# Performance work log

Hardware: AMD Instinct MI355X
Metric: run time of the kernel (lower is better)

The kernel has to match this reference:

```python
import jax, jax.numpy as jnp
import numpy as np

D = 1024  # encoder_output_size

def setup_inputs() -> dict:
    key = jax.random.key(0)
    ks = jax.random.split(key, 5)
    scale = 1.0 / np.sqrt(D)  # roughly matches nn.Linear init spread
    seq = jax.random.normal(ks[0], (2048, 8, D), dtype=jnp.float32)
    Kw1 = jax.random.normal(ks[1], (D, D), dtype=jnp.float32) * scale
    Kw2 = jax.random.normal(ks[2], (D, D), dtype=jnp.float32) * scale
    Qw1 = jax.random.normal(ks[3], (D, D), dtype=jnp.float32) * scale
    Qw2 = jax.random.normal(ks[4], (D, D), dtype=jnp.float32) * scale
    return {"sequence": seq, "Kw1": Kw1, "Kw2": Kw2, "Qw1": Qw1, "Qw2": Qw2}

def _mlp(x, W1, W2):
    # nn.Linear(bias=False): y = x @ W^T ; tanh after each
    return jnp.tanh(jnp.tanh(x @ W1.T) @ W2.T)

def reference(sequence, Kw1, Kw2, Qw1, Qw2):
    x = jnp.transpose(sequence, (1, 0, 2))          # [B, S, D]
    keys = _mlp(x, Kw1, Kw2)                        # [B, S, D]
    queries = _mlp(x, Qw1, Qw2)                     # [B, S, D]
    scale = 1.0 / jnp.sqrt(jnp.float32(x.shape[-1]))
    weights = jnp.einsum('bsd,btd->bst', keys, queries) * scale  # [B, S, S]
    weights = jax.nn.softmax(weights, axis=-1)
    attended = jnp.einsum('bst,btd->bsd', weights, x)            # [B, S, D]
    return jnp.transpose(attended, (1, 0, 2))       # [S, B, D]
```

## Files before the change

### kernel.cpp

```cpp
#include <hip/hip_runtime.h>
#include <hip/hip_bf16.h>

#define SEQ 2048
#define NB 8
#define DIM 1024

typedef __attribute__((ext_vector_type(4))) float f32x4;
typedef __attribute__((ext_vector_type(8))) short bf16x8;
typedef __attribute__((ext_vector_type(4))) unsigned short u16x4;

__device__ __forceinline__ unsigned short f2bf(float f) {
    __hip_bfloat16 h = __float2bfloat16(f);
    return *reinterpret_cast<unsigned short*>(&h);
}
__device__ __forceinline__ float bf2f(unsigned short u) {
    union { unsigned u; float f; } x; x.u = ((unsigned)u) << 16;
    return x.f;
}
__device__ __forceinline__ float fast_tanh(float x) {
    float e = __expf(x + x);
    float r = __builtin_amdgcn_rcpf(e + 1.0f);
    return fmaf(-2.0f, r, 1.0f);
}

__global__ __launch_bounds__(256) void convert_w4(const float* __restrict__ kw1,
                                                  const float* __restrict__ kw2,
                                                  const float* __restrict__ qw1,
                                                  const float* __restrict__ qw2,
                                                  unsigned short* __restrict__ out) {
    int sel = blockIdx.y;
    const float* src = sel == 0 ? kw1 : (sel == 1 ? qw1 : (sel == 2 ? kw2 : qw2));
    int i = blockIdx.x * 256 + threadIdx.x;
    float4 v = reinterpret_cast<const float4*>(src)[i];
    u16x4 o = { f2bf(v.x), f2bf(v.y), f2bf(v.z), f2bf(v.w) };
    reinterpret_cast<u16x4*>(out + (size_t)sel * DIM * DIM)[i] = o;
}

__global__ __launch_bounds__(256) void make_xb(const float* __restrict__ seq,
                                               unsigned short* __restrict__ xb) {
    int sb = blockIdx.x;
    int s = sb >> 3, b = sb & 7;
    const float4* src = reinterpret_cast<const float4*>(seq + (size_t)sb * DIM);
    u16x4* dst = reinterpret_cast<u16x4*>(xb + ((size_t)b * SEQ + s) * DIM);
    int t = threadIdx.x;
    float4 v = src[t];
    u16x4 o = { f2bf(v.x), f2bf(v.y), f2bf(v.z), f2bf(v.w) };
    dst[t] = o;
}

__global__ __launch_bounds__(256) void make_xbT(const float* __restrict__ seq,
                                                unsigned short* __restrict__ xbT) {
    __shared__ unsigned short tile[64][65];
    int s0 = blockIdx.x * 64, d0 = blockIdx.y * 64, b = blockIdx.z;
    int t = threadIdx.x;
    int dx = (t & 15) * 4, sy = t >> 4;
    #pragma unroll
    for (int i = 0; i < 4; ++i) {
        int s = s0 + sy + i * 16;
        float4 v = *reinterpret_cast<const float4*>(seq + ((size_t)s * NB + b) * DIM + d0 + dx);
        tile[sy + i * 16][dx + 0] = f2bf(v.x);
        tile[sy + i * 16][dx + 1] = f2bf(v.y);
        tile[sy + i * 16][dx + 2] = f2bf(v.z);
        tile[sy + i * 16][dx + 3] = f2bf(v.w);
    }
    __syncthreads();
    int sx = (t & 15) * 4, dy = t >> 4;
    #pragma unroll
    for (int i = 0; i < 4; ++i) {
        int d = d0 + dy + i * 16;
        u16x4 o = { tile[sx + 0][dy + i * 16], tile[sx + 1][dy + i * 16],
                    tile[sx + 2][dy + i * 16], tile[sx + 3][dy + i * 16] };
        *reinterpret_cast<u16x4*>(xbT + ((size_t)b * DIM + d) * SEQ + s0 + sx) = o;
    }
}

__global__ __launch_bounds__(256) void zero_rowsum(float* __restrict__ rs) {
    rs[blockIdx.x * 256 + threadIdx.x] = 0.0f;
}

__device__ __forceinline__ void gload16(const unsigned short* g, unsigned short* l) {
    __builtin_amdgcn_global_load_lds((const __attribute__((address_space(1))) void*)g,
                                     (__attribute__((address_space(3))) void*)l,
                                     16, 0, 0);
}

#define MFMA16(I0, J0)                                                                            \
    _Pragma("unroll")                                                                             \
    for (int ks = 0; ks < 2; ++ks)                                                                \
        _Pragma("unroll")                                                                         \
        for (int ii = 0; ii < 4; ++ii)                                                            \
            _Pragma("unroll")                                                                     \
            for (int jj = 0; jj < 2; ++jj)                                                        \
                acc[I0 + ii][J0 + jj] = __builtin_amdgcn_mfma_f32_16x16x32_bf16(                   \
                    a[I0 + ii][ks], b[J0 + jj][ks], acc[I0 + ii][J0 + jj], 0, 0, 0);

template<int MODE>
__global__ __launch_bounds__(512, 2) void gemm256(
    const unsigned short* __restrict__ A, size_t sA, int lda,
    const unsigned short* __restrict__ B, size_t sB, int ldb,
    void* __restrict__ Cv, size_t sC, int ldc,
    int K, float scale, float* __restrict__ rowsum)
{
    __shared__ unsigned short AsF[2 * 2 * 8192];
    __shared__ unsigned short BsF[2 * 2 * 8192];

    const int gx = gridDim.x, gy = gridDim.y;
    const int nwg = gx * gy * gridDim.z;
    const int fid = blockIdx.x + gx * (blockIdx.y + gy * blockIdx.z);
    const int cpx = nwg >> 3;
    const int sw = (fid & 7) * cpx + (fid >> 3);
    const int bx = sw % gx;
    const int rem = sw / gx;
    const int by = rem % gy;
    const int bz = rem / gy;

    const unsigned short* Ab = A + sA * bz;
    const unsigned short* Bb = B + sB * bz;
    const int m0 = by * 256;
    const int n0 = bx * 256;

    const int t_ = threadIdx.x;
    const int lane = t_ & 63;
    const int w = t_ >> 6;
    const int wm = w >> 2;
    const int wn = w & 3;

    const int l3 = lane >> 3;
    const int g7 = lane & 7;
    const size_t h128a = (size_t)128 * lda, r8a = (size_t)8 * lda;
    const size_t h128b = (size_t)128 * ldb, r8b = (size_t)8 * ldb;
    const unsigned short* gA = Ab + (size_t)(m0 + w * 16 + l3) * lda + ((g7 ^ l3) << 3);
    const unsigned short* gB = Bb + (size_t)(n0 + w * 16 + l3) * ldb + ((g7 ^ l3) << 3);

    const int fr = lane & 15;
    const int hi4 = lane >> 4;
    const int off0 = fr * 64 + (((hi4) ^ g7) << 3);
    const int off1 = fr * 64 + (((4 + hi4) ^ g7) << 3);
    const int bno = (wn & 1) * 4096;
    const int wlds = w * 1024;

    f32x4 acc[8][4] = {};
    const int NT = K >> 6;

    gload16(gA, AsF + wlds);                     gload16(gA + r8a, AsF + wlds + 512);
    gload16(gA + h128a, AsF + 8192 + wlds);      gload16(gA + h128a + r8a, AsF + 8192 + wlds + 512);
    gload16(gB, BsF + wlds);                     gload16(gB + r8b, BsF + wlds + 512);
    gload16(gB + h128b, BsF + 8192 + wlds);      gload16(gB + h128b + r8b, BsF + 8192 + wlds + 512);
    {
        const unsigned short* gb1 = gB + 64;
        gload16(gb1, BsF + 16384 + wlds);                gload16(gb1 + r8b, BsF + 16384 + wlds + 512);
        gload16(gb1 + h128b, BsF + 16384 + 8192 + wlds); gload16(gb1 + h128b + r8b, BsF + 16384 + 8192 + wlds + 512);
    }
    asm volatile("s_waitcnt vmcnt(4)" ::: "memory");
    __builtin_amdgcn_s_barrier();

    const unsigned short* gA1 = gA + 64;
    const unsigned short* gB2 = gB + 128;

    for (int u = 0; u < NT; ++u) {
        const int bu = (u & 1) * 16384;
        const int bn = 16384 - bu;
        const unsigned short* pA = AsF + bu + wm * 8192;
        const unsigned short* pB = BsF + bu + (wn >> 1) * 8192 + bno;
        const bool pfA = (u + 1 < NT);
        const bool pfB = (u + 2 < NT);
        bf16x8 a[8][2], b[4][2];

        #pragma unroll
        for (int i = 0; i < 4; ++i) {
            a[i][0] = *(const bf16x8*)&pA[i * 1024 + off0];
            a[i][1] = *(const bf16x8*)&pA[i * 1024 + off1];
        }
        #pragma unroll
        for (int j = 0; j < 2; ++j) {
            b[j][0] = *(const bf16x8*)&pB[j * 1024 + off0];
            b[j][1] = *(const bf16x8*)&pB[j * 1024 + off1];
        }
        if (pfA) { gload16(gA1, AsF + bn + wlds); gload16(gA1 + r8a, AsF + bn + wlds + 512); }
        asm volatile("s_waitcnt lgkmcnt(8)" ::: "memory");
        __builtin_amdgcn_s_barrier();
        asm volatile("s_waitcnt lgkmcnt(0)" ::: "memory");
        __builtin_amdgcn_sched_barrier(0);
        __builtin_amdgcn_s_setprio(1);
        MFMA16(0, 0)
        __builtin_amdgcn_s_setprio(0);
        __builtin_amdgcn_s_barrier();

        #pragma unroll
        for (int j = 2; j < 4; ++j) {
            b[j][0] = *(const bf16x8*)&pB[j * 1024 + off0];
            b[j][1] = *(const bf16x8*)&pB[j * 1024 + off1];
        }
        if (pfA) { gload16(gA1 + h128a, AsF + bn + 8192 + wlds); gload16(gA1 + h128a + r8a, AsF + bn + 8192 + wlds + 512); }
        __builtin_amdgcn_s_barrier();
        asm volatile("s_waitcnt lgkmcnt(0)" ::: "memory");
        __builtin_amdgcn_sched_barrier(0);
        __builtin_amdgcn_s_setprio(1);
        MFMA16(0, 2)
        __builtin_amdgcn_s_setprio(0);
        __builtin_amdgcn_s_barrier();

        #pragma unroll
        for (int i = 4; i < 8; ++i) {
            a[i][0] = *(const bf16x8*)&pA[i * 1024 + off0];
            a[i][1] = *(const bf16x8*)&pA[i * 1024 + off1];
        }
        if (pfB) { gload16(gB2, BsF + bu + wlds); gload16(gB2 + r8b, BsF + bu + wlds + 512); }
        __builtin_amdgcn_s_barrier();
        asm volatile("s_waitcnt lgkmcnt(0)" ::: "memory");
        __builtin_amdgcn_sched_barrier(0);
        __builtin_amdgcn_s_setprio(1);
        MFMA16(4, 0)
        __builtin_amdgcn_s_setprio(0);
        __builtin_amdgcn_s_barrier();

        if (pfB) {
            gload16(gB2 + h128b, BsF + bu + 8192 + wlds);
            gload16(gB2 + h128b + r8b, BsF + bu + 8192 + wlds + 512);
            asm volatile("s_waitcnt vmcnt(4)" ::: "memory");
        } else {
            asm volatile("s_waitcnt vmcnt(0)" ::: "memory");
        }
        __builtin_amdgcn_s_barrier();
        __builtin_amdgcn_sched_barrier(0);
        __builtin_amdgcn_s_setprio(1);
        MFMA16(4, 2)
        __builtin_amdgcn_s_setprio(0);
        __builtin_amdgcn_s_barrier();

        gA1 += 64; gB2 += 64;
    }

    if (MODE == 0) {
        unsigned short* C = reinterpret_cast<unsigned short*>(Cv) + sC * bz;
        #pragma unroll
        for (int mi = 0; mi < 8; ++mi)
            #pragma unroll
            for (int ni = 0; ni < 4; ++ni)
                #pragma unroll
                for (int r = 0; r < 4; ++r) {
                    int row = m0 + wm * 128 + mi * 16 + hi4 * 4 + r;
                    int col = n0 + wn * 64 + ni * 16 + fr;
                    C[(size_t)row * ldc + col] = f2bf(fast_tanh(acc[mi][ni][r]));
                }
    } else if (MODE == 3) {
        unsigned short* C = reinterpret_cast<unsigned short*>(Cv) + sC * bz;
        #pragma unroll
        for (int mi = 0; mi < 8; ++mi)
            #pragma unroll
            for (int r = 0; r < 4; ++r) {
                int row = m0 + wm * 128 + mi * 16 + hi4 * 4 + r;
                float ps = 0.f;
                #pragma unroll
                for (int ni = 0; ni < 4; ++ni) {
                    unsigned short h = f2bf(__expf(acc[mi][ni][r] * scale));
                    C[(size_t)row * ldc + (n0 + wn * 64 + ni * 16 + fr)] = h;
                    ps += bf2f(h);
                }
                ps += __shfl_xor(ps, 1, 64);
                ps += __shfl_xor(ps, 2, 64);
                ps += __shfl_xor(ps, 4, 64);
                ps += __shfl_xor(ps, 8, 64);
                if (fr == 0) atomicAdd(&rowsum[(size_t)bz * SEQ + row], ps);
            }
    } else {
        float* C = reinterpret_cast<float*>(Cv) + sC * bz;
        #pragma unroll
        for (int mi = 0; mi < 8; ++mi)
            #pragma unroll
            for (int r = 0; r < 4; ++r) {
                int row = m0 + wm * 128 + mi * 16 + hi4 * 4 + r;
                float invs = 1.0f / rowsum[(size_t)bz * SEQ + row];
                #pragma unroll
                for (int ni = 0; ni < 4; ++ni) {
                    int col = n0 + wn * 64 + ni * 16 + fr;
                    C[(size_t)row * ldc + col] = acc[mi][ni][r] * invs;
                }
            }
    }
}

extern "C" void kernel_launch(void* const* d_in, const int* in_sizes, int n_in,
                              void* d_out, int out_size, void* d_ws, size_t ws_size,
                              hipStream_t stream) {
    const float* seq  = (const float*)d_in[0];
    const float* Kw1f = (const float*)d_in[1];
    const float* Kw2f = (const float*)d_in[2];
    const float* Qw1f = (const float*)d_in[3];
    const float* Qw2f = (const float*)d_in[4];
    float* out = (float*)d_out;

    char* ws = (char*)d_ws;
    const size_t MB = 1024 * 1024;
    unsigned short* W    = (unsigned short*)(ws);
    unsigned short* Wkq1 = W;
    unsigned short* Wk2s = W + 2 * (size_t)DIM * DIM;
    unsigned short* xb   = (unsigned short*)(ws + 8 * MB);
    unsigned short* hKQ  = (unsigned short*)(ws + 40 * MB);
    unsigned short* kq   = (unsigned short*)(ws + 104 * MB);
    unsigned short* P    = (unsigned short*)(ws + 8 * MB);
    unsigned short* xbT  = (unsigned short*)(ws + 72 * MB);
    float* rowsum        = (float*)(ws);

    convert_w4<<<dim3(DIM * DIM / 4 / 256, 4), 256, 0, stream>>>(Kw1f, Kw2f, Qw1f, Qw2f, W);
    make_xb<<<SEQ * NB, 256, 0, stream>>>(seq, xb);

    gemm256<0><<<dim3(2 * DIM / 256, (NB * SEQ) / 256, 1), 512, 0, stream>>>(
        xb, 0, DIM, Wkq1, 0, DIM, hKQ, 0, 2 * DIM, DIM, 1.0f, nullptr);

    gemm256<0><<<dim3(DIM / 256, (NB * SEQ) / 256, 2), 512, 0, stream>>>(
        hKQ, (size_t)DIM, 2 * DIM, Wk2s, (size_t)DIM * DIM, DIM,
        kq, (size_t)NB * SEQ * DIM, DIM, DIM, 1.0f, nullptr);

    zero_rowsum<<<NB * SEQ / 256, 256, 0, stream>>>(rowsum);
    make_xbT<<<dim3(SEQ / 64, DIM / 64, NB), 256, 0, stream>>>(seq, xbT);

    gemm256<3><<<dim3(SEQ / 256, SEQ / 256, NB), 512, 0, stream>>>(
        kq, (size_t)SEQ * DIM, DIM, kq + (size_t)NB * SEQ * DIM, (size_t)SEQ * DIM, DIM,
        P, (size_t)SEQ * SEQ, SEQ, DIM, 0.03125f, rowsum);

    gemm256<4><<<dim3(DIM / 256, SEQ / 256, NB), 512, 0, stream>>>(
        P, (size_t)SEQ * SEQ, SEQ, xbT, (size_t)DIM * SEQ, SEQ,
        out, (size_t)DIM, NB * DIM, SEQ, 1.0f, rowsum);
}
```

Baseline: 348.6 us.

## Switch GEMM inner product from 16x16x32 to 32x32x16 bf16 MFMA

Replaces the 16x16x32 MFMA tiling with 32x32x16 MFMA instructions. Each wave now holds 4x2 accumulators of 32x32 instead of 8x4 of 16x16, and the LDS fragment loads and swizzle offsets are recomputed for the 32-row layout. The epilogues are rewritten for the 32x32 output register mapping, with an extra shuffle step in the row-sum reduction. The aim is fewer MFMA issues and LDS reads per tile, since the larger instruction has higher operand reuse. The risk is LDS bank conflicts with the new access pattern and a less efficient store pattern in the epilogue.

New measurement: 372.9 us. 1.07x slower.

```diff
diff --git a/kernel.cpp b/kernel.cpp
--- a/kernel.cpp
+++ b/kernel.cpp
@@ -6,6 +6,7 @@
 #define DIM 1024
 
 typedef __attribute__((ext_vector_type(4))) float f32x4;
+typedef __attribute__((ext_vector_type(16))) float f32x16;
 typedef __attribute__((ext_vector_type(8))) short bf16x8;
 typedef __attribute__((ext_vector_type(4))) unsigned short u16x4;
 
@@ -84,15 +85,13 @@
                                      16, 0, 0);
 }
 
-#define MFMA16(I0, J0)                                                                            \
+#define MFMA8(MI0, NI)                                                                            \
     _Pragma("unroll")                                                                             \
-    for (int ks = 0; ks < 2; ++ks)                                                                \
+    for (int ks = 0; ks < 4; ++ks)                                                                \
         _Pragma("unroll")                                                                         \
-        for (int ii = 0; ii < 4; ++ii)                                                            \
-            _Pragma("unroll")                                                                     \
-            for (int jj = 0; jj < 2; ++jj)                                                        \
-                acc[I0 + ii][J0 + jj] = __builtin_amdgcn_mfma_f32_16x16x32_bf16(                   \
-                    a[I0 + ii][ks], b[J0 + jj][ks], acc[I0 + ii][J0 + jj], 0, 0, 0);
+        for (int d = 0; d < 2; ++d)                                                               \
+            acc[MI0 + d][NI] = __builtin_amdgcn_mfma_f32_32x32x16_bf16(                           \
+                a[MI0 + d][ks], b[NI][ks], acc[MI0 + d][NI], 0, 0, 0);
 
 template<int MODE>
 __global__ __launch_bounds__(512, 2) void gemm256(
@@ -132,14 +131,16 @@
     const unsigned short* gA = Ab + (size_t)(m0 + w * 16 + l3) * lda + ((g7 ^ l3) << 3);
     const unsigned short* gB = Bb + (size_t)(n0 + w * 16 + l3) * ldb + ((g7 ^ l3) << 3);
 
-    const int fr = lane & 15;
-    const int hi4 = lane >> 4;
-    const int off0 = fr * 64 + (((hi4) ^ g7) << 3);
-    const int off1 = fr * 64 + (((4 + hi4) ^ g7) << 3);
+    const int l31 = lane & 31;
+    const int l5 = lane >> 5;
+    int goff[4];
+    #pragma unroll
+    for (int ks = 0; ks < 4; ++ks) goff[ks] = (((ks * 2 + l5) ^ g7) << 3);
+    const int rbase = l31 * 64;
     const int bno = (wn & 1) * 4096;
     const int wlds = w * 1024;
 
-    f32x4 acc[8][4] = {};
+    f32x16 acc[4][2] = {};
     const int NT = K >> 6;
 
     gload16(gA, AsF + wlds);                     gload16(gA + r8a, AsF + wlds + 512);
@@ -164,53 +165,49 @@
         const unsigned short* pB = BsF + bu + (wn >> 1) * 8192 + bno;
         const bool pfA = (u + 1 < NT);
         const bool pfB = (u + 2 < NT);
-        bf16x8 a[8][2], b[4][2];
-
-        #pragma unroll
-        for (int i = 0; i < 4; ++i) {
-            a[i][0] = *(const bf16x8*)&pA[i * 1024 + off0];
-            a[i][1] = *(const bf16x8*)&pA[i * 1024 + off1];
+        bf16x8 a[4][4], b[2][4];
+
+        #pragma unroll
+        for (int ks = 0; ks < 4; ++ks) {
+            a[0][ks] = *(const bf16x8*)&pA[rbase + goff[ks]];
+            a[1][ks] = *(const bf16x8*)&pA[2048 + rbase + goff[ks]];
         }
         #pragma unroll
-        for (int j = 0; j < 2; ++j) {
-            b[j][0] = *(const bf16x8*)&pB[j * 1024 + off0];
-            b[j][1] = *(const bf16x8*)&pB[j * 1024 + off1];
-        }
+        for (int ks = 0; ks < 4; ++ks)
+            b[0][ks] = *(const bf16x8*)&pB[rbase + goff[ks]];
         if (pfA) { gload16(gA1, AsF + bn + wlds); gload16(gA1 + r8a, AsF + bn + wlds + 512); }
         asm volatile("s_waitcnt lgkmcnt(8)" ::: "memory");
         __builtin_amdgcn_s_barrier();
         asm volatile("s_waitcnt lgkmcnt(0)" ::: "memory");
         __builtin_amdgcn_sched_barrier(0);
         __builtin_amdgcn_s_setprio(1);
-        MFMA16(0, 0)
+        MFMA8(0, 0)
         __builtin_amdgcn_s_setprio(0);
         __builtin_amdgcn_s_barrier();
 
         #pragma unroll
-        for (int j = 2; j < 4; ++j) {
-            b[j][0] = *(const bf16x8*)&pB[j * 1024 + off0];
-            b[j][1] = *(const bf16x8*)&pB[j * 1024 + off1];
-        }
+        for (int ks = 0; ks < 4; ++ks)
+            b[1][ks] = *(const bf16x8*)&pB[2048 + rbase + goff[ks]];
         if (pfA) { gload16(gA1 + h128a, AsF + bn + 8192 + wlds); gload16(gA1 + h128a + r8a, AsF + bn + 8192 + wlds + 512); }
         __builtin_amdgcn_s_barrier();
         asm volatile("s_waitcnt lgkmcnt(0)" ::: "memory");
         __builtin_amdgcn_sched_barrier(0);
         __builtin_amdgcn_s_setprio(1);
-        MFMA16(0, 2)
+        MFMA8(0, 1)
         __builtin_amdgcn_s_setprio(0);
         __builtin_amdgcn_s_barrier();
 
         #pragma unroll
-        for (int i = 4; i < 8; ++i) {
-            a[i][0] = *(const bf16x8*)&pA[i * 1024 + off0];
-            a[i][1] = *(const bf16x8*)&pA[i * 1024 + off1];
+        for (int ks = 0; ks < 4; ++ks) {
+            a[2][ks] = *(const bf16x8*)&pA[4096 + rbase + goff[ks]];
+            a[3][ks] = *(const bf16x8*)&pA[6144 + rbase + goff[ks]];
         }
         if (pfB) { gload16(gB2, BsF + bu + wlds); gload16(gB2 + r8b, BsF + bu + wlds + 512); }
         __builtin_amdgcn_s_barrier();
         asm volatile("s_waitcnt lgkmcnt(0)" ::: "memory");
         __builtin_amdgcn_sched_barrier(0);
         __builtin_amdgcn_s_setprio(1);
-        MFMA16(4, 0)
+        MFMA8(2, 0)
         __builtin_amdgcn_s_setprio(0);
         __builtin_amdgcn_s_barrier();
 
@@ -224,7 +221,7 @@
         __builtin_amdgcn_s_barrier();
         __builtin_amdgcn_sched_barrier(0);
         __builtin_amdgcn_s_setprio(1);
-        MFMA16(4, 2)
+        MFMA8(2, 1)
         __builtin_amdgcn_s_setprio(0);
         __builtin_amdgcn_s_barrier();
 
@@ -234,47 +231,48 @@
     if (MODE == 0) {
         unsigned short* C = reinterpret_cast<unsigned short*>(Cv) + sC * bz;
         #pragma unroll
-        for (int mi = 0; mi < 8; ++mi)
+        for (int mi = 0; mi < 4; ++mi)
             #pragma unroll
-            for (int ni = 0; ni < 4; ++ni)
+            for (int ni = 0; ni < 2; ++ni)
                 #pragma unroll
-                for (int r = 0; r < 4; ++r) {
-                    int row = m0 + wm * 128 + mi * 16 + hi4 * 4 + r;
-                    int col = n0 + wn * 64 + ni * 16 + fr;
-                    C[(size_t)row * ldc + col] = f2bf(fast_tanh(acc[mi][ni][r]));
+                for (int rg = 0; rg < 16; ++rg) {
+                    int row = m0 + wm * 128 + mi * 32 + (rg & 3) + 8 * (rg >> 2) + 4 * l5;
+                    int col = n0 + wn * 64 + ni * 32 + l31;
+                    C[(size_t)row * ldc + col] = f2bf(fast_tanh(acc[mi][ni][rg]));
                 }
     } else if (MODE == 3) {
         unsigned short* C = reinterpret_cast<unsigned short*>(Cv) + sC * bz;
         #pragma unroll
-        for (int mi = 0; mi < 8; ++mi)
+        for (int mi = 0; mi < 4; ++mi)
             #pragma unroll
-            for (int r = 0; r < 4; ++r) {
-                int row = m0 + wm * 128 + mi * 16 + hi4 * 4 + r;
+            for (int rg = 0; rg < 16; ++rg) {
+                int row = m0 + wm * 128 + mi * 32 + (rg & 3) + 8 * (rg >> 2) + 4 * l5;
                 float ps = 0.f;
                 #pragma unroll
-                for (int ni = 0; ni < 4; ++ni) {
-                    unsigned short h = f2bf(__expf(acc[mi][ni][r] * scale));
-                    C[(size_t)row * ldc + (n0 + wn * 64 + ni * 16 + fr)] = h;
+                for (int ni = 0; ni < 2; ++ni) {
+                    unsigned short h = f2bf(__expf(acc[mi][ni][rg] * scale));
+                    C[(size_t)row * ldc + (n0 + wn * 64 + ni * 32 + l31)] = h;
                     ps += bf2f(h);
                 }
                 ps += __shfl_xor(ps, 1, 64);
                 ps += __shfl_xor(ps, 2, 64);
                 ps += __shfl_xor(ps, 4, 64);
                 ps += __shfl_xor(ps, 8, 64);
-                if (fr == 0) atomicAdd(&rowsum[(size_t)bz * SEQ + row], ps);
+                ps += __shfl_xor(ps, 16, 64);
+                if (l31 == 0) atomicAdd(&rowsum[(size_t)bz * SEQ + row], ps);
             }
     } else {
         float* C = reinterpret_cast<float*>(Cv) + sC * bz;
         #pragma unroll
-        for (int mi = 0; mi < 8; ++mi)
+        for (int mi = 0; mi < 4; ++mi)
             #pragma unroll
-            for (int r = 0; r < 4; ++r) {
-                int row = m0 + wm * 128 + mi * 16 + hi4 * 4 + r;
+            for (int rg = 0; rg < 16; ++rg) {
+                int row = m0 + wm * 128 + mi * 32 + (rg & 3) + 8 * (rg >> 2) + 4 * l5;
                 float invs = 1.0f / rowsum[(size_t)bz * SEQ + row];
                 #pragma unroll
-                for (int ni = 0; ni < 4; ++ni) {
-                    int col = n0 + wn * 64 + ni * 16 + fr;
-                    C[(size_t)row * ldc + col] = acc[mi][ni][r] * invs;
+                for (int ni = 0; ni < 2; ++ni) {
+                    int col = n0 + wn * 64 + ni * 32 + l31;
+                    C[(size_t)row * ldc + col] = acc[mi][ni][rg] * invs;
                 }
             }
     }
```
